# Optimization experiments

Hardware: AMD Instinct MI355X
Metric: run time of the kernel (lower is better)

The kernel has to match this reference:

```python
import jax, jax.numpy as jnp
import numpy as np

N_HEADS = 4
LN_EPS = 1e-3  # keras LayerNormalization default epsilon


def setup_inputs() -> dict:
    key = jax.random.key(0)
    ks = jax.random.split(key, 9)
    B, S, D = 4, 2048, 128
    w = 0.08  # ~glorot scale for D=128
    return {
        "x": jax.random.normal(ks[0], (B, S, D), jnp.float32),
        "Wq": jax.random.normal(ks[1], (D, D), jnp.float32) * w,
        "bq": jnp.zeros((D,), jnp.float32),
        "Wk": jax.random.normal(ks[2], (D, D), jnp.float32) * w,
        "bk": jnp.zeros((D,), jnp.float32),
        "Wv": jax.random.normal(ks[3], (D, D), jnp.float32) * w,
        "bv": jnp.zeros((D,), jnp.float32),
        "Wu": jax.random.normal(ks[4], (D, 2 * D), jnp.float32) * w,
        "bu": jnp.zeros((2 * D,), jnp.float32),
        "pos_w": jax.random.normal(ks[5], (2 * S - 1,), jnp.float32) * 0.02,
        "ln_gamma": 1.0 + jax.random.normal(ks[6], (2 * D,), jnp.float32) * 0.3,
        "ln_beta": jax.random.normal(ks[7], (2 * D,), jnp.float32) * 1e-4,
        "Wf": jax.random.normal(ks[8], (2 * D, D), jnp.float32) * w,
        "bf": jnp.zeros((D,), jnp.float32),
    }


def reference(x, Wq, bq, Wk, bk, Wv, bv, Wu, bu, pos_w, ln_gamma, ln_beta, Wf, bf):
    B, S, D = x.shape
    H = N_HEADS
    hd = D // H

    # q/k/v DNNs: single Dense with silu activation (activations=["silu"])
    q = jax.nn.silu(x @ Wq + bq)
    k = jax.nn.silu(x @ Wk + bk)
    v = jax.nn.silu(x @ Wv + bv)
    u = x @ Wu + bu  # [B,S,2D], u_proj has no activation

    # relative position bias: bias[i, j] = pos_w[(S-1) + j - i]  (offset = 0)
    idx = (S - 1) + jnp.arange(S)[None, :] - jnp.arange(S)[:, None]
    rel = pos_w[idx]  # [S, S]
    pos_attn = jnp.einsum('nm,bmd->bnd', rel, v)  # [B,S,D]

    # multi-head self-attention with squared-masked-SiLU scores
    qh = q.reshape(B, S, H, hd).transpose(0, 2, 1, 3)
    kh = k.reshape(B, S, H, hd).transpose(0, 2, 1, 3)
    vh = v.reshape(B, S, H, hd).transpose(0, 2, 1, 3)
    scores = jnp.einsum('bhnd,bhmd->bhnm', qh, kh) / jnp.sqrt(jnp.float32(hd))
    causal = jnp.tril(jnp.ones((S, S), dtype=bool))  # band_part(-1, 0)
    # original: scores *= where(mask==1, scores, 0)  ->  scores^2 inside mask, 0 outside
    scores = jnp.where(causal[None, None], scores * scores, 0.0)
    self_attn = jnp.einsum('bhnm,bhmd->bhnd', jax.nn.silu(scores), vh)
    self_attn = self_attn.transpose(0, 2, 1, 3).reshape(B, S, D)

    a = jnp.concatenate([self_attn, pos_attn], axis=-1)  # [B,S,2D]
    mu = jnp.mean(a, axis=-1, keepdims=True)
    var = jnp.mean(jnp.square(a - mu), axis=-1, keepdims=True)
    a = (a - mu) * jax.lax.rsqrt(var + LN_EPS) * ln_gamma + ln_beta

    out = jax.nn.relu((u * a) @ Wf + bf) + x
    return out
```

## Files before the change

kernel.cpp:

```cpp
#include <hip/hip_runtime.h>
#include <hip/hip_bf16.h>

#define B 4
#define S 2048
#define D 128
#define H 4
#define HD 32
#define D2 256
#define BSD (B*S*D)

#define LDK 40
#define LDV 72
#define LDSC 72
#define LDX 136

typedef __attribute__((ext_vector_type(8))) short bf16x8;
typedef __attribute__((ext_vector_type(4))) short bf16x4;
typedef __attribute__((ext_vector_type(4))) float f32x4;

__device__ __forceinline__ float silu_f(float z){ return z / (1.f + __expf(-z)); }
__device__ __forceinline__ short f2bfs(float f){
    __hip_bfloat16 h = __float2bfloat16(f);
    return *reinterpret_cast<short*>(&h);
}
__device__ __forceinline__ float bfs2f(short s){
    __hip_bfloat16 h = *reinterpret_cast<__hip_bfloat16*>(&s);
    return __bfloat162float(h);
}

__global__ __launch_bounds__(256) void k_wt(
    const float* __restrict__ Wq, const float* __restrict__ Wk,
    const float* __restrict__ Wv, const float* __restrict__ Wu,
    const float* __restrict__ Wf,
    short* __restrict__ wqt, short* __restrict__ wkt, short* __restrict__ wvt,
    short* __restrict__ wut, short* __restrict__ wft)
{
    int e = blockIdx.x * 256 + threadIdx.x;
    if (e < 16384) { int n = e >> 7, k = e & 127; wqt[e] = f2bfs(Wq[k * D  + n]); return; }
    e -= 16384;
    if (e < 16384) { int n = e >> 7, k = e & 127; wkt[e] = f2bfs(Wk[k * D  + n]); return; }
    e -= 16384;
    if (e < 16384) { int n = e >> 7, k = e & 127; wvt[e] = f2bfs(Wv[k * D  + n]); return; }
    e -= 16384;
    if (e < 32768) { int n = e >> 7, k = e & 127; wut[e] = f2bfs(Wu[k * D2 + n]); return; }
    e -= 32768;
    { int n = e >> 8, k = e & 255; wft[e] = f2bfs(Wf[k * D + n]); }
}

__global__ __launch_bounds__(256) void k_qkvu(
    const float* __restrict__ x,
    const short* __restrict__ wqt, const short* __restrict__ wkt,
    const short* __restrict__ wvt, const short* __restrict__ wut,
    const float* __restrict__ bq, const float* __restrict__ bk,
    const float* __restrict__ bv, const float* __restrict__ bu,
    short* __restrict__ qb, short* __restrict__ kb, short* __restrict__ vtb,
    short* __restrict__ ub)
{
    __shared__ short xs[64 * LDX] __attribute__((aligned(16)));
    const int rt = blockIdx.x;
    const int cs = blockIdx.y;
    const int row0 = rt * 64;
    const int tid  = threadIdx.x;
    const int w    = tid >> 6;
    const int lane = tid & 63;
    const int q16  = lane >> 4;
    const int l15  = lane & 15;

    const short* WT; const float* bias; int cn0; int kind;
    if (cs < 2)      { WT = wqt; bias = bq; cn0 = cs * 64;       kind = 0; }
    else if (cs < 4) { WT = wkt; bias = bk; cn0 = (cs - 2) * 64; kind = 1; }
    else if (cs < 6) { WT = wvt; bias = bv; cn0 = (cs - 4) * 64; kind = 2; }
    else             { WT = wut; bias = bu; cn0 = (cs - 6) * 64; kind = 3; }

    #pragma unroll
    for (int i = 0; i < 8; ++i) {
        int e = tid + i * 256;
        int row = e >> 5, c4 = (e & 31) * 4;
        f32x4 xv = *(const f32x4*)(x + (row0 + row) * D + c4);
        short tmp[4];
        #pragma unroll
        for (int j = 0; j < 4; ++j) tmp[j] = f2bfs(xv[j]);
        *(bf16x4*)(xs + row * LDX + c4) = *(bf16x4*)tmp;
    }
    __syncthreads();

    f32x4 acc[4];
    #pragma unroll
    for (int ct = 0; ct < 4; ++ct) acc[ct] = (f32x4){0.f, 0.f, 0.f, 0.f};
    #pragma unroll
    for (int ks = 0; ks < 4; ++ks) {
        bf16x8 af = *(const bf16x8*)(xs + (w * 16 + l15) * LDX + ks * 32 + q16 * 8);
        #pragma unroll
        for (int ct = 0; ct < 4; ++ct) {
            bf16x8 bfr = *(const bf16x8*)(WT + (cn0 + ct * 16 + l15) * D + ks * 32 + q16 * 8);
            acc[ct] = __builtin_amdgcn_mfma_f32_16x16x32_bf16(af, bfr, acc[ct], 0, 0, 0);
        }
    }

    const int bb   = row0 / S;
    const int mloc = (row0 % S) + w * 16 + q16 * 4;
    #pragma unroll
    for (int ct = 0; ct < 4; ++ct) {
        const int c  = ct * 16 + l15;
        const float bcol = bias[cn0 + c];
        if (kind == 2) {
            short tmp[4];
            #pragma unroll
            for (int r = 0; r < 4; ++r) tmp[r] = f2bfs(silu_f(acc[ct][r] + bcol));
            *(bf16x4*)(vtb + (bb * D + cn0 + c) * S + mloc) = *(bf16x4*)tmp;
        } else if (kind == 3) {
            #pragma unroll
            for (int r = 0; r < 4; ++r)
                ub[(row0 + w * 16 + q16 * 4 + r) * D2 + cn0 + c] = f2bfs(acc[ct][r] + bcol);
        } else {
            short* dst = (kind == 0) ? qb : kb;
            #pragma unroll
            for (int r = 0; r < 4; ++r)
                dst[(row0 + w * 16 + q16 * 4 + r) * D + cn0 + c] = f2bfs(silu_f(acc[ct][r] + bcol));
        }
    }
}

__global__ __launch_bounds__(256) void k_mix(
    const short* __restrict__ qb, const short* __restrict__ kb,
    const short* __restrict__ vtb, const float* __restrict__ pos_w,
    float* __restrict__ as_part, float* __restrict__ ap)
{
    __shared__ char smem[20544] __attribute__((aligned(16)));
    const int tid  = threadIdx.x;
    const int w    = tid >> 6;
    const int lane = tid & 63;
    const int q16  = lane >> 4;
    const int l15  = lane & 15;
    const int bid  = blockIdx.x;

    if (bid < 1024) {
        short* ks  = (short*)smem;
        short* vt  = (short*)(smem + 5120);
        short* scw = (short*)(smem + 9728) + w * 16 * LDSC;
        const int att = bid;
        const int nt  = 31 - (att >> 5);
        const int sub = att & 31;
        const int h   = sub & 3;
        const int b   = (sub >> 2) & 3;
        const int zz  = sub >> 4;
        const int n0  = nt * 64;

        bf16x8 qfrag = *(const bf16x8*)(qb + (b * S + n0 + w * 16 + l15) * D + h * HD + q16 * 8);
        f32x4 o0 = {0.f, 0.f, 0.f, 0.f};
        f32x4 o1 = {0.f, 0.f, 0.f, 0.f};

        const int nm    = nt + 1;
        const int half1 = (nm + 1) >> 1;
        const int it_lo = zz ? half1 : 0;
        const int it_hi = zz ? nm : half1;

        for (int it = it_lo; it < it_hi; ++it) {
            const int m0 = it * 64;
            __syncthreads();
            {
                int row = tid >> 2, c8 = tid & 3;
                *(bf16x8*)(ks + row * LDK + c8 * 8) =
                    *(const bf16x8*)(kb + (b * S + m0 + row) * D + h * HD + c8 * 8);
                int d = tid >> 3, m8 = tid & 7;
                *(bf16x8*)(vt + d * LDV + m8 * 8) =
                    *(const bf16x8*)(vtb + (b * D + h * HD + d) * S + m0 + m8 * 8);
            }
            __syncthreads();
            const int n_gb = n0 + w * 16 + q16 * 4;
            #pragma unroll
            for (int t = 0; t < 4; ++t) {
                bf16x8 kf = *(const bf16x8*)(ks + (t * 16 + l15) * LDK + q16 * 8);
                f32x4 sacc = {0.f, 0.f, 0.f, 0.f};
                sacc = __builtin_amdgcn_mfma_f32_16x16x32_bf16(qfrag, kf, sacc, 0, 0, 0);
                const int m_g = m0 + t * 16 + l15;
                #pragma unroll
                for (int r = 0; r < 4; ++r) {
                    float sv = sacc[r] * 0.17677669529663687f;
                    float x2 = sv * sv;
                    float wgt = silu_f(x2);
                    if (m_g > n_gb + r) wgt = 0.f;
                    scw[(q16 * 4 + r) * LDSC + t * 16 + l15] = f2bfs(wgt);
                }
            }
            #pragma unroll
            for (int kt = 0; kt < 2; ++kt) {
                bf16x8 pf = *(const bf16x8*)(scw + l15 * LDSC + kt * 32 + q16 * 8);
                bf16x8 v0 = *(const bf16x8*)(vt + l15 * LDV        + kt * 32 + q16 * 8);
                bf16x8 v1 = *(const bf16x8*)(vt + (16 + l15) * LDV + kt * 32 + q16 * 8);
                o0 = __builtin_amdgcn_mfma_f32_16x16x32_bf16(pf, v0, o0, 0, 0, 0);
                o1 = __builtin_amdgcn_mfma_f32_16x16x32_bf16(pf, v1, o1, 0, 0, 0);
            }
        }
        float* dst = as_part + zz * BSD;
        const int nrow = n0 + w * 16 + q16 * 4;
        #pragma unroll
        for (int r = 0; r < 4; ++r) {
            dst[(b * S + nrow + r) * D + h * HD + l15]      = o0[r];
            dst[(b * S + nrow + r) * D + h * HD + 16 + l15] = o1[r];
        }
    } else {
        short* pw = (short*)smem;
        short* vt = (short*)(smem + 2112);
        const int pid = bid - 1024;
        const int n0  = (pid >> 3) * 32;
        const int sub = pid & 7;
        const int b   = sub >> 1;
        const int z   = sub & 1;
        const int s   = w >> 1;
        const int dh  = w & 1;

        const int base_g = 2016 + z * 1024 - n0;
        for (int i = tid; i < 1055; i += 256) pw[i] = f2bfs(pos_w[base_g + i]);

        f32x4 acc[4];
        #pragma unroll
        for (int dt = 0; dt < 4; ++dt) acc[dt] = (f32x4){0.f, 0.f, 0.f, 0.f};

        for (int mt = 0; mt < 16; ++mt) {
            __syncthreads();
            #pragma unroll
            for (int i = 0; i < 4; ++i) {
                int e = tid + i * 256;
                int d = e >> 3, m8 = e & 7;
                *(bf16x8*)(vt + d * LDV + m8 * 8) =
                    *(const bf16x8*)(vtb + (b * D + d) * S + z * 1024 + mt * 64 + m8 * 8);
            }
            __syncthreads();
            #pragma unroll
            for (int kt = 0; kt < 2; ++kt) {
                bf16x8 af;
                int idx0 = mt * 64 + kt * 32 + q16 * 8 + 31 - s * 16 - l15;
                #pragma unroll
                for (int j = 0; j < 8; ++j) af[j] = pw[idx0 + j];
                #pragma unroll
                for (int dt = 0; dt < 4; ++dt) {
                    bf16x8 bv = *(const bf16x8*)(vt + (dh * 64 + dt * 16 + l15) * LDV + kt * 32 + q16 * 8);
                    acc[dt] = __builtin_amdgcn_mfma_f32_16x16x32_bf16(af, bv, acc[dt], 0, 0, 0);
                }
            }
        }
        float* dst = ap + z * BSD;
        const int nrow = n0 + s * 16 + q16 * 4;
        #pragma unroll
        for (int dt = 0; dt < 4; ++dt)
            #pragma unroll
            for (int r = 0; r < 4; ++r)
                dst[(b * S + nrow + r) * D + dh * 64 + dt * 16 + l15] = acc[dt][r];
    }
}

__global__ __launch_bounds__(256) void k_final(
    const float* __restrict__ as_part, const float* __restrict__ ap,
    const short* __restrict__ ub, const short* __restrict__ wft,
    const float* __restrict__ gamma, const float* __restrict__ beta,
    const float* __restrict__ bfb,
    const float* __restrict__ x, float* __restrict__ out)
{
    __shared__ float hs[8][264];
    __shared__ float red[8][4][2];
    __shared__ float part[2][8][D];
    const int tid  = threadIdx.x;
    const int row0 = blockIdx.x * 8;
    const int wave = tid >> 6, lane = tid & 63;
    const float gam = gamma[tid];
    const float bet = beta[tid];

    float av[8];
    #pragma unroll
    for (int r = 0; r < 8; ++r) {
        const int row = row0 + r;
        float v_;
        if (tid < 128) v_ = as_part[row * D + tid] + as_part[BSD + row * D + tid];
        else           v_ = ap[row * D + (tid - 128)] + ap[BSD + row * D + (tid - 128)];
        av[r] = v_;
        float s1 = v_, s2 = v_ * v_;
        #pragma unroll
        for (int off = 32; off > 0; off >>= 1) {
            s1 += __shfl_down(s1, off);
            s2 += __shfl_down(s2, off);
        }
        if (lane == 0) { red[r][wave][0] = s1; red[r][wave][1] = s2; }
    }
    __syncthreads();
    #pragma unroll
    for (int r = 0; r < 8; ++r) {
        float sum = red[r][0][0] + red[r][1][0] + red[r][2][0] + red[r][3][0];
        float sq  = red[r][0][1] + red[r][1][1] + red[r][2][1] + red[r][3][1];
        float mu  = sum * (1.f / 256.f);
        float var = sq * (1.f / 256.f) - mu * mu;
        float rs  = rsqrtf(var + 1e-3f);
        float an  = (av[r] - mu) * rs * gam + bet;
        hs[r][tid] = bfs2f(ub[(row0 + r) * D2 + tid]) * an;
    }
    __syncthreads();

    const int d = tid & 127, half = tid >> 7;
    float acc[8] = {0.f, 0.f, 0.f, 0.f, 0.f, 0.f, 0.f, 0.f};
    for (int j8 = 0; j8 < 16; ++j8) {
        bf16x8 wv = *(const bf16x8*)(wft + d * D2 + half * 128 + j8 * 8);
        float wf_[8];
        #pragma unroll
        for (int j = 0; j < 8; ++j) wf_[j] = bfs2f(wv[j]);
        #pragma unroll
        for (int r = 0; r < 8; ++r) {
            const float* hp = &hs[r][half * 128 + j8 * 8];
            f32x4 h0 = *(const f32x4*)(hp);
            f32x4 h1 = *(const f32x4*)(hp + 4);
            acc[r] += h0[0]*wf_[0] + h0[1]*wf_[1] + h0[2]*wf_[2] + h0[3]*wf_[3]
                    + h1[0]*wf_[4] + h1[1]*wf_[5] + h1[2]*wf_[6] + h1[3]*wf_[7];
        }
    }
    #pragma unroll
    for (int r = 0; r < 8; ++r) part[half][r][d] = acc[r];
    __syncthreads();
    if (half == 0) {
        float bfv = bfb[d];
        #pragma unroll
        for (int r = 0; r < 8; ++r) {
            int row = row0 + r;
            float o = part[0][r][d] + part[1][r][d] + bfv;
            o = fmaxf(o, 0.f);
            o += x[row * D + d];
            out[row * D + d] = o;
        }
    }
}

extern "C" void kernel_launch(void* const* d_in, const int* in_sizes, int n_in,
                              void* d_out, int out_size, void* d_ws, size_t ws_size,
                              hipStream_t stream)
{
    const float* x     = (const float*)d_in[0];
    const float* Wq    = (const float*)d_in[1];
    const float* bq    = (const float*)d_in[2];
    const float* Wk    = (const float*)d_in[3];
    const float* bk    = (const float*)d_in[4];
    const float* Wv    = (const float*)d_in[5];
    const float* bv    = (const float*)d_in[6];
    const float* Wu    = (const float*)d_in[7];
    const float* bu    = (const float*)d_in[8];
    const float* pos_w = (const float*)d_in[9];
    const float* gamma = (const float*)d_in[10];
    const float* beta  = (const float*)d_in[11];
    const float* Wf    = (const float*)d_in[12];
    const float* bfb   = (const float*)d_in[13];
    float* out = (float*)d_out;

    char* p = (char*)d_ws;
    short* qb      = (short*)p;  p += (size_t)BSD * 2;
    short* kb      = (short*)p;  p += (size_t)BSD * 2;
    short* vtb     = (short*)p;  p += (size_t)BSD * 2;
    short* ubuf    = (short*)p;  p += (size_t)2 * BSD * 2;
    float* as_part = (float*)p;  p += (size_t)2 * BSD * 4;
    float* ap      = (float*)p;  p += (size_t)2 * BSD * 4;
    short* wqt     = (short*)p;  p += (size_t)D * D * 2;
    short* wkt     = (short*)p;  p += (size_t)D * D * 2;
    short* wvt     = (short*)p;  p += (size_t)D * D * 2;
    short* wut     = (short*)p;  p += (size_t)D2 * D * 2;
    short* wft     = (short*)p;  p += (size_t)D * D2 * 2;

    k_wt   <<<dim3(448),     256, 0, stream>>>(Wq, Wk, Wv, Wu, Wf, wqt, wkt, wvt, wut, wft);
    k_qkvu <<<dim3(128, 10), 256, 0, stream>>>(x, wqt, wkt, wvt, wut, bq, bk, bv, bu, qb, kb, vtb, ubuf);
    k_mix  <<<dim3(1536),    256, 0, stream>>>(qb, kb, vtb, pos_w, as_part, ap);
    k_final<<<dim3(1024),    256, 0, stream>>>(as_part, ap, ubuf, wft, gamma, beta, bfb, x, out);
}
```

Baseline: 156.2 us.

## Use MFMA for final projection and reload x once per row tile in qkvu

The final kernel swaps its scalar FP32 dot-product loop for bf16 MFMA 16x16x32 over 16-row tiles, with LayerNorm done by 16 lanes per row and shuffle-xor reductions, and h stored to LDS as bf16. The qkvu kernel changes from a 2D grid, where each x tile was loaded and converted 10 times, to one block per 16 rows that computes all 640 output columns from a single x load. This removes the redundant x reads and the slow scalar FMA loop, at the cost of bf16 rounding of the u*a product and fewer, larger blocks.

```diff
diff --git a/kernel.cpp b/kernel.cpp
--- a/kernel.cpp
+++ b/kernel.cpp
@@ -13,6 +13,7 @@
 #define LDV 72
 #define LDSC 72
 #define LDX 136
+#define LDH 264
 
 typedef __attribute__((ext_vector_type(8))) short bf16x8;
 typedef __attribute__((ext_vector_type(4))) short bf16x4;
@@ -56,26 +57,18 @@
     short* __restrict__ qb, short* __restrict__ kb, short* __restrict__ vtb,
     short* __restrict__ ub)
 {
-    __shared__ short xs[64 * LDX] __attribute__((aligned(16)));
-    const int rt = blockIdx.x;
-    const int cs = blockIdx.y;
-    const int row0 = rt * 64;
+    __shared__ short xs[16 * LDX] __attribute__((aligned(16)));
+    const int row0 = blockIdx.x * 16;
     const int tid  = threadIdx.x;
     const int w    = tid >> 6;
     const int lane = tid & 63;
     const int q16  = lane >> 4;
     const int l15  = lane & 15;
 
-    const short* WT; const float* bias; int cn0; int kind;
-    if (cs < 2)      { WT = wqt; bias = bq; cn0 = cs * 64;       kind = 0; }
-    else if (cs < 4) { WT = wkt; bias = bk; cn0 = (cs - 2) * 64; kind = 1; }
-    else if (cs < 6) { WT = wvt; bias = bv; cn0 = (cs - 4) * 64; kind = 2; }
-    else             { WT = wut; bias = bu; cn0 = (cs - 6) * 64; kind = 3; }
-
-    #pragma unroll
-    for (int i = 0; i < 8; ++i) {
-        int e = tid + i * 256;
-        int row = e >> 5, c4 = (e & 31) * 4;
+    #pragma unroll
+    for (int i = 0; i < 2; ++i) {
+        int quad = tid + i * 256;
+        int row = quad >> 5, c4 = (quad & 31) * 4;
         f32x4 xv = *(const f32x4*)(x + (row0 + row) * D + c4);
         short tmp[4];
         #pragma unroll
@@ -84,39 +77,44 @@
     }
     __syncthreads();
 
-    f32x4 acc[4];
-    #pragma unroll
-    for (int ct = 0; ct < 4; ++ct) acc[ct] = (f32x4){0.f, 0.f, 0.f, 0.f};
-    #pragma unroll
-    for (int ks = 0; ks < 4; ++ks) {
-        bf16x8 af = *(const bf16x8*)(xs + (w * 16 + l15) * LDX + ks * 32 + q16 * 8);
-        #pragma unroll
-        for (int ct = 0; ct < 4; ++ct) {
-            bf16x8 bfr = *(const bf16x8*)(WT + (cn0 + ct * 16 + l15) * D + ks * 32 + q16 * 8);
-            acc[ct] = __builtin_amdgcn_mfma_f32_16x16x32_bf16(af, bfr, acc[ct], 0, 0, 0);
-        }
-    }
+    bf16x8 af[4];
+    #pragma unroll
+    for (int ks = 0; ks < 4; ++ks)
+        af[ks] = *(const bf16x8*)(xs + l15 * LDX + ks * 32 + q16 * 8);
 
     const int bb   = row0 / S;
-    const int mloc = (row0 % S) + w * 16 + q16 * 4;
-    #pragma unroll
-    for (int ct = 0; ct < 4; ++ct) {
-        const int c  = ct * 16 + l15;
-        const float bcol = bias[cn0 + c];
+    const int mloc = (row0 % S) + q16 * 4;
+
+    #pragma unroll
+    for (int t = 0; t < 10; ++t) {
+        const int g = w * 160 + t * 16;
+        const short* WT; const float* bias; int base; int kind;
+        if (g < 128)      { WT = wqt; bias = bq; base = 0;   kind = 0; }
+        else if (g < 256) { WT = wkt; bias = bk; base = 128; kind = 1; }
+        else if (g < 384) { WT = wvt; bias = bv; base = 256; kind = 2; }
+        else              { WT = wut; bias = bu; base = 384; kind = 3; }
+        const int nloc = g - base;
+        f32x4 acc = {0.f, 0.f, 0.f, 0.f};
+        #pragma unroll
+        for (int ks = 0; ks < 4; ++ks) {
+            bf16x8 bfr = *(const bf16x8*)(WT + (nloc + l15) * D + ks * 32 + q16 * 8);
+            acc = __builtin_amdgcn_mfma_f32_16x16x32_bf16(af[ks], bfr, acc, 0, 0, 0);
+        }
+        const float bcol = bias[nloc + l15];
         if (kind == 2) {
             short tmp[4];
             #pragma unroll
-            for (int r = 0; r < 4; ++r) tmp[r] = f2bfs(silu_f(acc[ct][r] + bcol));
-            *(bf16x4*)(vtb + (bb * D + cn0 + c) * S + mloc) = *(bf16x4*)tmp;
+            for (int r = 0; r < 4; ++r) tmp[r] = f2bfs(silu_f(acc[r] + bcol));
+            *(bf16x4*)(vtb + (bb * D + nloc + l15) * S + mloc) = *(bf16x4*)tmp;
         } else if (kind == 3) {
             #pragma unroll
             for (int r = 0; r < 4; ++r)
-                ub[(row0 + w * 16 + q16 * 4 + r) * D2 + cn0 + c] = f2bfs(acc[ct][r] + bcol);
+                ub[(row0 + q16 * 4 + r) * D2 + nloc + l15] = f2bfs(acc[r] + bcol);
         } else {
             short* dst = (kind == 0) ? qb : kb;
             #pragma unroll
             for (int r = 0; r < 4; ++r)
-                dst[(row0 + w * 16 + q16 * 4 + r) * D + cn0 + c] = f2bfs(silu_f(acc[ct][r] + bcol));
+                dst[(row0 + q16 * 4 + r) * D + nloc + l15] = f2bfs(silu_f(acc[r] + bcol));
         }
     }
 }
@@ -257,72 +255,71 @@
     const float* __restrict__ bfb,
     const float* __restrict__ x, float* __restrict__ out)
 {
-    __shared__ float hs[8][264];
-    __shared__ float red[8][4][2];
-    __shared__ float part[2][8][D];
+    __shared__ short hsb[16 * LDH] __attribute__((aligned(16)));
     const int tid  = threadIdx.x;
-    const int row0 = blockIdx.x * 8;
-    const int wave = tid >> 6, lane = tid & 63;
-    const float gam = gamma[tid];
-    const float bet = beta[tid];
-
-    float av[8];
-    #pragma unroll
-    for (int r = 0; r < 8; ++r) {
-        const int row = row0 + r;
-        float v_;
-        if (tid < 128) v_ = as_part[row * D + tid] + as_part[BSD + row * D + tid];
-        else           v_ = ap[row * D + (tid - 128)] + ap[BSD + row * D + (tid - 128)];
-        av[r] = v_;
-        float s1 = v_, s2 = v_ * v_;
-        #pragma unroll
-        for (int off = 32; off > 0; off >>= 1) {
-            s1 += __shfl_down(s1, off);
-            s2 += __shfl_down(s2, off);
-        }
-        if (lane == 0) { red[r][wave][0] = s1; red[r][wave][1] = s2; }
+    const int row0 = blockIdx.x * 16;
+
+    {
+        const int row = tid >> 4;
+        const int c   = tid & 15;
+        float av[16];
+        float s1 = 0.f, s2 = 0.f;
+        #pragma unroll
+        for (int j = 0; j < 16; ++j) {
+            int col = c + j * 16;
+            float v_;
+            if (col < 128) v_ = as_part[(row0 + row) * D + col] + as_part[BSD + (row0 + row) * D + col];
+            else           v_ = ap[(row0 + row) * D + col - 128] + ap[BSD + (row0 + row) * D + col - 128];
+            av[j] = v_;
+            s1 += v_;
+            s2 += v_ * v_;
+        }
+        #pragma unroll
+        for (int off = 1; off < 16; off <<= 1) {
+            s1 += __shfl_xor(s1, off);
+            s2 += __shfl_xor(s2, off);
+        }
+        float mu  = s1 * (1.f / 256.f);
+        float var = s2 * (1.f / 256.f) - mu * mu;
+        float rs  = rsqrtf(var + 1e-3f);
+        #pragma unroll
+        for (int j = 0; j < 16; ++j) {
+            int col = c + j * 16;
+            float an = (av[j] - mu) * rs * gamma[col] + beta[col];
+            float h  = bfs2f(ub[(row0 + row) * D2 + col]) * an;
+            hsb[row * LDH + col] = f2bfs(h);
+        }
     }
     __syncthreads();
-    #pragma unroll
-    for (int r = 0; r < 8; ++r) {
-        float sum = red[r][0][0] + red[r][1][0] + red[r][2][0] + red[r][3][0];
-        float sq  = red[r][0][1] + red[r][1][1] + red[r][2][1] + red[r][3][1];
-        float mu  = sum * (1.f / 256.f);
-        float var = sq * (1.f / 256.f) - mu * mu;
-        float rs  = rsqrtf(var + 1e-3f);
-        float an  = (av[r] - mu) * rs * gam + bet;
-        hs[r][tid] = bfs2f(ub[(row0 + r) * D2 + tid]) * an;
-    }
-    __syncthreads();
-
-    const int d = tid & 127, half = tid >> 7;
-    float acc[8] = {0.f, 0.f, 0.f, 0.f, 0.f, 0.f, 0.f, 0.f};
-    for (int j8 = 0; j8 < 16; ++j8) {
-        bf16x8 wv = *(const bf16x8*)(wft + d * D2 + half * 128 + j8 * 8);
-        float wf_[8];
-        #pragma unroll
-        for (int j = 0; j < 8; ++j) wf_[j] = bfs2f(wv[j]);
-        #pragma unroll
-        for (int r = 0; r < 8; ++r) {
-            const float* hp = &hs[r][half * 128 + j8 * 8];
-            f32x4 h0 = *(const f32x4*)(hp);
-            f32x4 h1 = *(const f32x4*)(hp + 4);
-            acc[r] += h0[0]*wf_[0] + h0[1]*wf_[1] + h0[2]*wf_[2] + h0[3]*wf_[3]
-                    + h1[0]*wf_[4] + h1[1]*wf_[5] + h1[2]*wf_[6] + h1[3]*wf_[7];
-        }
-    }
-    #pragma unroll
-    for (int r = 0; r < 8; ++r) part[half][r][d] = acc[r];
-    __syncthreads();
-    if (half == 0) {
-        float bfv = bfb[d];
-        #pragma unroll
-        for (int r = 0; r < 8; ++r) {
-            int row = row0 + r;
-            float o = part[0][r][d] + part[1][r][d] + bfv;
-            o = fmaxf(o, 0.f);
-            o += x[row * D + d];
-            out[row * D + d] = o;
+
+    const int w    = tid >> 6;
+    const int lane = tid & 63;
+    const int q16  = lane >> 4;
+    const int l15  = lane & 15;
+    f32x4 o[2];
+    o[0] = (f32x4){0.f, 0.f, 0.f, 0.f};
+    o[1] = (f32x4){0.f, 0.f, 0.f, 0.f};
+    #pragma unroll
+    for (int ks = 0; ks < 8; ++ks) {
+        bf16x8 af = *(const bf16x8*)(hsb + l15 * LDH + ks * 32 + q16 * 8);
+        #pragma unroll
+        for (int ci = 0; ci < 2; ++ci) {
+            const int ct = w * 2 + ci;
+            bf16x8 bfr = *(const bf16x8*)(wft + (ct * 16 + l15) * D2 + ks * 32 + q16 * 8);
+            o[ci] = __builtin_amdgcn_mfma_f32_16x16x32_bf16(af, bfr, o[ci], 0, 0, 0);
+        }
+    }
+    #pragma unroll
+    for (int ci = 0; ci < 2; ++ci) {
+        const int n = (w * 2 + ci) * 16 + l15;
+        const float bfv = bfb[n];
+        #pragma unroll
+        for (int r = 0; r < 4; ++r) {
+            const int row = row0 + q16 * 4 + r;
+            float oo = o[ci][r] + bfv;
+            oo = fmaxf(oo, 0.f);
+            oo += x[row * D + n];
+            out[row * D + n] = oo;
         }
     }
 }
@@ -360,8 +357,8 @@
     short* wut     = (short*)p;  p += (size_t)D2 * D * 2;
     short* wft     = (short*)p;  p += (size_t)D * D2 * 2;
 
-    k_wt   <<<dim3(448),     256, 0, stream>>>(Wq, Wk, Wv, Wu, Wf, wqt, wkt, wvt, wut, wft);
-    k_qkvu <<<dim3(128, 10), 256, 0, stream>>>(x, wqt, wkt, wvt, wut, bq, bk, bv, bu, qb, kb, vtb, ubuf);
-    k_mix  <<<dim3(1536),    256, 0, stream>>>(qb, kb, vtb, pos_w, as_part, ap);
-    k_final<<<dim3(1024),    256, 0, stream>>>(as_part, ap, ubuf, wft, gamma, beta, bfb, x, out);
-}
+    k_wt   <<<dim3(448),  256, 0, stream>>>(Wq, Wk, Wv, Wu, Wf, wqt, wkt, wvt, wut, wft);
+    k_qkvu <<<dim3(512),  256, 0, stream>>>(x, wqt, wkt, wvt, wut, bq, bk, bv, bu, qb, kb, vtb, ubuf);
+    k_mix  <<<dim3(1536), 256, 0, stream>>>(qb, kb, vtb, pos_w, as_part, ap);
+    k_final<<<dim3(512),  256, 0, stream>>>(as_part, ap, ubuf, wft, gamma, beta, bfb, x, out);
+}
```

New measurement: 143.4 us. -8.2%, faster.
